# Performance work log

Measured on AMD Instinct MI355X. Metric: run time of the kernel, lower is better.

The kernel has to match this reference:

```python
import jax, jax.numpy as jnp
import numpy as np

NUM_HEADS = 16
NUM_KV_HEADS = 4
ROPE_BASE = 10000.0
TRAIN_SEQ_LEN = 2048


def _rms_norm(x):
    eps = jnp.asarray(jnp.finfo(x.dtype).eps, x.dtype)
    return x * jax.lax.rsqrt(jnp.mean(x * x, axis=-1, keepdims=True) + eps)


def _rope_cos_sin(seq_len, head_dim, dtype):
    # seq_len <= TRAIN_SEQ_LEN -> no NTK rescaling, matches Rotary buffer path
    half = head_dim // 2
    inv_freq = 1.0 / (ROPE_BASE ** (jnp.arange(0, head_dim, 2, dtype=jnp.float32) / head_dim))
    t = jnp.arange(seq_len, dtype=jnp.float32)
    freqs = jnp.outer(t, inv_freq)  # [S, half]
    cos = jnp.cos(freqs)[None, :, None, :].astype(dtype)
    sin = jnp.sin(freqs)[None, :, None, :].astype(dtype)
    return cos, sin


def _apply_rotary(x, cos, sin):
    half = x.shape[-1] // 2
    x1, x2 = x[..., :half], x[..., half:]
    return jnp.concatenate([x1 * cos + x2 * sin, -x1 * sin + x2 * cos], axis=-1)


def setup_inputs() -> dict:
    key = jax.random.key(0)
    ks = jax.random.split(key, 5)
    B, S, D = 2, 2048, 2048
    kv_dim = NUM_KV_HEADS * (D // NUM_HEADS)
    sw = 0.02
    return {
        "x": jax.random.normal(ks[0], (B, S, D), jnp.float32),
        "Wq": jax.random.normal(ks[1], (D, D), jnp.float32) * sw,
        "Wk": jax.random.normal(ks[2], (kv_dim, D), jnp.float32) * sw,
        "Wv": jax.random.normal(ks[3], (kv_dim, D), jnp.float32) * sw,
        "Wproj": jax.random.normal(ks[4], (D, D), jnp.float32) * sw,
        "q_gain": jnp.ones((NUM_HEADS,), jnp.float32),
    }


def reference(x, Wq, Wk, Wv, Wproj, q_gain):
    B, S, D = x.shape
    H, Hkv = NUM_HEADS, NUM_KV_HEADS
    hd = D // H
    r = H // Hkv

    q = (x @ Wq.T).reshape(B, S, H, hd)
    k = (x @ Wk.T).reshape(B, S, Hkv, hd)
    v = (x @ Wv.T).reshape(B, S, Hkv, hd)

    q = _rms_norm(q)
    k = _rms_norm(k)

    cos, sin = _rope_cos_sin(S, hd, q.dtype)
    q = _apply_rotary(q, cos, sin)
    k = _apply_rotary(k, cos, sin)
    q = q * q_gain.astype(q.dtype)[None, None, :, None]

    # GQA: repeat kv heads (repeat_interleave along head dim)
    k = jnp.repeat(k, r, axis=2)  # [B,S,H,hd]
    v = jnp.repeat(v, r, axis=2)

    scale = 1.0 / jnp.sqrt(jnp.asarray(hd, q.dtype))
    scores = jnp.einsum("bqhd,bkhd->bhqk", q, k) * scale
    causal = jnp.tril(jnp.ones((S, S), dtype=bool))
    scores = jnp.where(causal[None, None], scores, jnp.asarray(-jnp.inf, scores.dtype))
    attn = jax.nn.softmax(scores, axis=-1)
    y = jnp.einsum("bhqk,bkhd->bqhd", attn, v)

    return y.reshape(B, S, D) @ Wproj.T
```

## Files before the change

kernel.cpp:

```cpp
#include <hip/hip_runtime.h>

#define D_MODEL 2048
#define SEQ 2048
#define BATCH 2
#define NH 16
#define NKV 4
#define HD 128
#define KVD (NKV * HD)
#define QKVN (D_MODEL + 2 * KVD)
#define MROWS (BATCH * SEQ)

typedef __attribute__((ext_vector_type(8))) short short8;
typedef __attribute__((ext_vector_type(4))) float f32x4;

__device__ __forceinline__ unsigned short f2bf(float f) {
    union { float f; unsigned int u; } v; v.f = f;
    unsigned int r = (v.u + 0x7FFFu + ((v.u >> 16) & 1u)) >> 16;
    return (unsigned short)r;
}

__device__ __forceinline__ unsigned short f2bf_pos(float f) {
    union { float f; unsigned int u; } v; v.f = f;
    return (unsigned short)((v.u + 0x8000u) >> 16);
}

__device__ __forceinline__ float bf2f(unsigned short u) {
    union { float f; unsigned int i; } v; v.i = ((unsigned int)u) << 16;
    return v.f;
}

__device__ __forceinline__ void async16(const void* g, void* l) {
    __builtin_amdgcn_global_load_lds((const __attribute__((address_space(1))) void*)g,
                                     (__attribute__((address_space(3))) void*)l, 16, 0, 0);
}

__global__ __launch_bounds__(256) void cast_all(const float* __restrict__ x,
                                                const float* __restrict__ wq,
                                                const float* __restrict__ wk,
                                                const float* __restrict__ wv,
                                                const float* __restrict__ wp,
                                                unsigned short* __restrict__ xb,
                                                unsigned short* __restrict__ wqkv,
                                                unsigned short* __restrict__ wpb) {
    int i = blockIdx.x * 256 + threadIdx.x;
    const float4* s; ushort4* d; int j;
    if (i < 2097152)      { s = (const float4*)x;  d = (ushort4*)xb;             j = i; }
    else if (i < 3145728) { s = (const float4*)wq; d = (ushort4*)wqkv;           j = i - 2097152; }
    else if (i < 3407872) { s = (const float4*)wk; d = (ushort4*)wqkv + 1048576; j = i - 3145728; }
    else if (i < 3670016) { s = (const float4*)wv; d = (ushort4*)wqkv + 1310720; j = i - 3407872; }
    else                  { s = (const float4*)wp; d = (ushort4*)wpb;            j = i - 3670016; }
    float4 v = s[j];
    ushort4 o;
    o.x = f2bf(v.x); o.y = f2bf(v.y); o.z = f2bf(v.z); o.w = f2bf(v.w);
    d[j] = o;
}

__global__ __launch_bounds__(512) void gemm_qkv(const unsigned short* __restrict__ A,
                                                const unsigned short* __restrict__ W,
                                                const float* __restrict__ gain,
                                                unsigned short* __restrict__ qbuf,
                                                unsigned short* __restrict__ kbuf,
                                                unsigned short* __restrict__ vtb) {
    __shared__ unsigned short smem[65536];
    unsigned short* tile = smem;
    const int K = D_MODEL;
    const int tid  = threadIdx.x;
    const int lane = tid & 63;
    const int wave = tid >> 6;
    const int qm   = lane & 15;
    const int quad = lane >> 4;
    const int wr   = wave >> 2;
    const int wc   = wave & 3;
    const int lin = blockIdx.x + 12 * blockIdx.y;
    const int l2  = (lin & 7) * 24 + (lin >> 3);
    const int bx  = l2 % 12;
    const int m0  = (l2 / 12) * 256;
    const int n0 = bx * 256;

    f32x4 acc[2][2][4][2];
#pragma unroll
    for (int a = 0; a < 2; a++)
#pragma unroll
        for (int b = 0; b < 2; b++)
#pragma unroll
            for (int c = 0; c < 4; c++)
#pragma unroll
                for (int d = 0; d < 2; d++) acc[a][b][c][d] = (f32x4){0.f, 0.f, 0.f, 0.f};

    const unsigned short* Asrc = A + (size_t)(m0 + (tid >> 3)) * K + (((tid & 7) ^ ((tid >> 3) & 7)) * 8);
    const unsigned short* Bsrc = W + (size_t)(n0 + (tid >> 3)) * K + (((tid & 7) ^ ((tid >> 3) & 7)) * 8);
    const int dstg = tid * 8;
    const int ck0 = ((quad ^ (qm & 7)) * 8);
    const int ck1 = (((4 + quad) ^ (qm & 7)) * 8);
    const int arow = wr * 64 + qm;
    const int brow = wc * 32 + qm;

    short8 af[4][2], bf0[2][2], bf1[2][2];

#define STG_A(mh, bufv, kt1) \
    async16(Asrc + (size_t)((mh) * 128) * K + (kt1),      &smem[(bufv) * 16384 + (mh) * 8192 + dstg]); \
    async16(Asrc + (size_t)((mh) * 128 + 64) * K + (kt1), &smem[(bufv) * 16384 + (mh) * 8192 + 4096 + dstg]);
#define STG_B(nh, bufv, kt1) \
    async16(Bsrc + (size_t)((nh) * 128) * K + (kt1),      &smem[32768 + (bufv) * 16384 + (nh) * 8192 + dstg]); \
    async16(Bsrc + (size_t)((nh) * 128 + 64) * K + (kt1), &smem[32768 + (bufv) * 16384 + (nh) * 8192 + 4096 + dstg]);

#define RD_A(ab, mh) { \
    _Pragma("unroll") \
    for (int m = 0; m < 4; m++) { \
        af[m][0] = *(const short8*)&smem[(ab) + ((mh) * 128 + arow + m * 16) * 64 + ck0]; \
        af[m][1] = *(const short8*)&smem[(ab) + ((mh) * 128 + arow + m * 16) * 64 + ck1]; \
    } }
#define RD_B(bb, nh, dstf) { \
    _Pragma("unroll") \
    for (int n = 0; n < 2; n++) { \
        dstf[n][0] = *(const short8*)&smem[(bb) + ((nh) * 128 + brow + n * 16) * 64 + ck0]; \
        dstf[n][1] = *(const short8*)&smem[(bb) + ((nh) * 128 + brow + n * 16) * 64 + ck1]; \
    } }
#define MFMA16(mh, nh, bfr) { \
    __builtin_amdgcn_s_setprio(1); \
    _Pragma("unroll") \
    for (int m = 0; m < 4; m++) \
        _Pragma("unroll") \
        for (int n = 0; n < 2; n++) { \
            acc[mh][nh][m][n] = __builtin_amdgcn_mfma_f32_16x16x32_bf16(af[m][0], bfr[n][0], acc[mh][nh][m][n], 0, 0, 0); \
            acc[mh][nh][m][n] = __builtin_amdgcn_mfma_f32_16x16x32_bf16(af[m][1], bfr[n][1], acc[mh][nh][m][n], 0, 0, 0); \
        } \
    __builtin_amdgcn_s_setprio(0); }

#define BARv asm volatile("s_barrier" ::: "memory")
#define WV4  asm volatile("s_waitcnt vmcnt(4)" ::: "memory")
#define WV2  asm volatile("s_waitcnt vmcnt(2)" ::: "memory")
#define WV0  asm volatile("s_waitcnt vmcnt(0)" ::: "memory")

#define STEP(p, kt1) { \
     RD_A((p)*16384, 0) RD_B(32768 + (p)*16384, 0, bf0) STG_A(0, (p)^1, kt1) \
    BARv; MFMA16(0, 0, bf0) WV4; BARv; \
     RD_B(32768 + (p)*16384, 1, bf1) STG_B(0, (p)^1, kt1) \
    BARv; MFMA16(0, 1, bf1) WV4; BARv; \
     RD_A((p)*16384, 1) STG_B(1, (p)^1, kt1) \
    BARv; MFMA16(1, 0, bf0) BARv; \
     STG_A(1, (p)^1, kt1) \
    BARv; MFMA16(1, 1, bf1) WV4; BARv; \
}
#define STEPE(p) { \
    RD_A((p)*16384, 0) RD_B(32768 + (p)*16384, 0, bf0) BARv; MFMA16(0, 0, bf0) WV2; BARv; \
    RD_B(32768 + (p)*16384, 1, bf1)                    BARv; MFMA16(0, 1, bf1) WV0; BARv; \
    RD_A((p)*16384, 1)                                 BARv; MFMA16(1, 0, bf0) BARv; \
    MFMA16(1, 1, bf1) \
}

    STG_A(0, 0, 0) STG_B(0, 0, 0) STG_B(1, 0, 0) STG_A(1, 0, 0)
    WV4; BARv;

#pragma unroll 1
    for (int t2 = 0; t2 < 15; ++t2) {
        STEP(0, t2 * 128 + 64)
        STEP(1, t2 * 128 + 128)
    }
    STEP(0, 1984)
    STEPE(1)
#undef STG_A
#undef STG_B
#undef RD_A
#undef RD_B
#undef MFMA16
#undef STEP
#undef STEPE

    const int s_base = m0 & 2047;
    const int bb = m0 >> 11;
    const float invf = __builtin_amdgcn_exp2f(-(float)lane * 0.20761871f - 2.6514961f);

#pragma unroll
    for (int half = 0; half < 2; ++half) {
        __syncthreads();
#pragma unroll
        for (int nh = 0; nh < 2; nh++)
#pragma unroll
            for (int m = 0; m < 4; m++)
#pragma unroll
                for (int n = 0; n < 2; n++)
#pragma unroll
                    for (int r = 0; r < 4; r++) {
                        int row = wr * 64 + m * 16 + quad * 4 + r;
                        int col = nh * 128 + wc * 32 + n * 16 + qm;
                        tile[row * 264 + col] = f2bf(acc[half][nh][m][n][r]);
                    }
        __syncthreads();

        if (bx < 10) {
            const bool isq = bx < 8;
#pragma unroll
            for (int hh = 0; hh < 2; hh++) {
                const int h = (isq ? 2 * bx : (bx - 8) * 2) + hh;
                const float g = isq ? gain[h] * 0.12751744f : 1.0f;
                unsigned short* dst = isq
                    ? qbuf + ((size_t)(bb * NH + h) * SEQ + s_base + half * 128) * HD
                    : kbuf + ((size_t)(bb * NKV + h) * SEQ + s_base + half * 128) * HD;
                for (int rr = 0; rr < 16; rr++) {
                    int row = wave * 16 + rr;
                    float x1 = bf2f(tile[row * 264 + hh * 128 + lane]);
                    float x2 = bf2f(tile[row * 264 + hh * 128 + 64 + lane]);
                    float ss = x1 * x1 + x2 * x2;
                    ss += __shfl_xor(ss, 1);  ss += __shfl_xor(ss, 2);  ss += __shfl_xor(ss, 4);
                    ss += __shfl_xor(ss, 8);  ss += __shfl_xor(ss, 16); ss += __shfl_xor(ss, 32);
                    float rs = rsqrtf(ss * (1.0f / 128.0f) + 1.1920929e-07f);
                    float rev = (float)(s_base + half * 128 + row) * invf;
                    rev -= truncf(rev);
                    float sn = __builtin_amdgcn_sinf(rev);
                    float cs = __builtin_amdgcn_cosf(rev);
                    float a1 = x1 * rs, a2 = x2 * rs;
                    float o1 = (a1 * cs + a2 * sn) * g;
                    float o2 = (a2 * cs - a1 * sn) * g;
                    dst[(size_t)row * HD + lane]      = f2bf(o1);
                    dst[(size_t)row * HD + 64 + lane] = f2bf(o2);
                }
            }
        } else {
            const int sc = (tid & 31) * 4;
            const int d0 = tid >> 5;
#pragma unroll
            for (int hh = 0; hh < 2; hh++) {
                const int hk = (bx - 10) * 2 + hh;
                unsigned short* dstv = vtb + ((size_t)(bb * NKV + hk) * HD) * SEQ + s_base + half * 128;
#pragma unroll
                for (int i = 0; i < 8; i++) {
                    int d = d0 + 16 * i;
                    ushort4 ov;
                    ov.x = tile[(sc + 0) * 264 + hh * 128 + d];
                    ov.y = tile[(sc + 1) * 264 + hh * 128 + d];
                    ov.z = tile[(sc + 2) * 264 + hh * 128 + d];
                    ov.w = tile[(sc + 3) * 264 + hh * 128 + d];
                    *(ushort4*)(dstv + (size_t)d * SEQ + sc) = ov;
                }
            }
        }
    }
}

__global__ __launch_bounds__(256) void gemm_bt(const unsigned short* __restrict__ A,
                                               const unsigned short* __restrict__ W,
                                               float* __restrict__ C, int M, int N, int K) {
    __shared__ unsigned short smem[32768];
    unsigned short* Al = smem;
    unsigned short* Bl = smem + 16384;
    const int tid  = threadIdx.x;
    const int lane = tid & 63;
    const int wave = tid >> 6;
    const int qm   = lane & 15;
    const int quad = lane >> 4;
    const int m0 = blockIdx.y * 128;
    const int n0 = blockIdx.x * 128;
    const int wm = (wave >> 1) * 64;
    const int wn = (wave & 1) * 64;

    f32x4 acc[4][4];
#pragma unroll
    for (int i = 0; i < 4; i++)
#pragma unroll
        for (int j = 0; j < 4; j++) acc[i][j] = (f32x4){0.f, 0.f, 0.f, 0.f};

    const int r1 = tid >> 2;
    const int c1 = (((tid & 3) ^ ((tid >> 3) & 3)) * 8);
    const unsigned short* Ag = A + (size_t)(m0 + r1) * K + c1;
    const unsigned short* Wg = W + (size_t)(n0 + r1) * K + c1;
    const int stg = wave * 512;
    const int swq = ((qm >> 1) & 3) * 8;

#define STG_B2(khv, bufv) \
    async16(Ag + (khv) * 32,                  &Al[(bufv) * 8192 + (khv) * 4096 + stg]); \
    async16(Ag + (khv) * 32 + (size_t)64 * K, &Al[(bufv) * 8192 + (khv) * 4096 + 2048 + stg]); \
    async16(Wg + (khv) * 32,                  &Bl[(bufv) * 8192 + (khv) * 4096 + stg]); \
    async16(Wg + (khv) * 32 + (size_t)64 * K, &Bl[(bufv) * 8192 + (khv) * 4096 + 2048 + stg]);

#define CMP_B2(bufv, khv) { \
    short8 af[4], bfr[4]; \
    _Pragma("unroll") \
    for (int i = 0; i < 4; i++) { \
        af[i]  = *(const short8*)&Al[(bufv) * 8192 + (khv) * 4096 + (wm + i * 16 + qm) * 32 + (quad * 8 ^ swq)]; \
        bfr[i] = *(const short8*)&Bl[(bufv) * 8192 + (khv) * 4096 + (wn + i * 16 + qm) * 32 + (quad * 8 ^ swq)]; \
    } \
    __builtin_amdgcn_s_setprio(1); \
    _Pragma("unroll") \
    for (int mi = 0; mi < 4; mi++) \
        _Pragma("unroll") \
        for (int ni = 0; ni < 4; ni++) \
            acc[mi][ni] = __builtin_amdgcn_mfma_f32_16x16x32_bf16(af[mi], bfr[ni], acc[mi][ni], 0, 0, 0); \
    __builtin_amdgcn_s_setprio(0); \
}

    STG_B2(0, 0)
    STG_B2(1, 0)
    Ag += 64; Wg += 64;
    asm volatile("s_waitcnt vmcnt(4)\n\ts_barrier" ::: "memory");

    int buf = 0;
    for (int t = 0; t < K / 64 - 1; ++t) {
        STG_B2(0, buf ^ 1)
        CMP_B2(buf, 0)
        asm volatile("s_waitcnt vmcnt(4)\n\ts_barrier" ::: "memory");
        STG_B2(1, buf ^ 1)
        CMP_B2(buf, 1)
        asm volatile("s_waitcnt vmcnt(4)\n\ts_barrier" ::: "memory");
        Ag += 64; Wg += 64;
        buf ^= 1;
    }
    CMP_B2(buf, 0)
    asm volatile("s_waitcnt vmcnt(0)\n\ts_barrier" ::: "memory");
    CMP_B2(buf, 1)
#undef STG_B2
#undef CMP_B2

#pragma unroll
    for (int mi = 0; mi < 4; mi++) {
#pragma unroll
        for (int r = 0; r < 4; r++) {
            int row = m0 + wm + mi * 16 + quad * 4 + r;
            float* Crow = C + (size_t)row * N + n0 + wn + qm;
#pragma unroll
            for (int ni = 0; ni < 4; ni++) Crow[ni * 16] = acc[mi][ni][r];
        }
    }
}

__global__ __launch_bounds__(256, 4) void attn(const unsigned short* __restrict__ qb,
                                               const unsigned short* __restrict__ kb,
                                               const unsigned short* __restrict__ vt,
                                               const float* __restrict__ gain,
                                               unsigned short* __restrict__ y) {
    __shared__ unsigned short Ks[8192];
    __shared__ unsigned short Vs[8192];
    __shared__ unsigned short plds[4][1024];
    const int tid  = threadIdx.x;
    const int lane = tid & 63;
    const int wave = tid >> 6;
    const int bh   = blockIdx.x & 31;
    const int g4   = blockIdx.x >> 5;
    const int gg = g4 & 7;
    const int gs = g4 >> 3;
    const int qt64 = (gs == 0) ? gg : (gs == 1) ? (31 - gg) : (gs == 2) ? (8 + gg) : (23 - gg);
    const int h = bh & 15;
    const int b = bh >> 4;
    const int qm   = lane & 15;
    const int quad = lane >> 4;
    const int q0    = qt64 * 64;
    const int qrow0 = q0 + wave * 16;
    const float M = 17.0f * fabsf(gain[h]);

    const unsigned short* Qp = qb + (((size_t)(b * NH + h)) * SEQ + qrow0) * HD;
    const unsigned short* Kp = kb + ((size_t)(b * NKV + (h >> 2))) * SEQ * HD;
    const unsigned short* Vp = vt + ((size_t)(b * NKV + (h >> 2))) * HD * SEQ;

    short8 qf[4];
#pragma unroll
    for (int c = 0; c < 4; c++)
        qf[c] = *(const short8*)(Qp + qm * HD + c * 32 + quad * 8);

    f32x4 o[8];
#pragma unroll
    for (int t = 0; t < 8; t++) o[t] = (f32x4){0.f, 0.f, 0.f, 0.f};
    float lr[4] = {0.f, 0.f, 0.f, 0.f};

    const unsigned short* KsA = Kp + (size_t)(tid >> 4) * HD + (((tid & 15) ^ (tid >> 4)) & 15) * 8;
    const unsigned short* VsA = Vp + (size_t)(tid >> 3) * SEQ + (((tid & 7) ^ ((tid >> 3) & 7)) * 8);
    char* KsB = (char*)Ks + wave * 1024;
    char* VsB = (char*)Vs + wave * 1024;
    unsigned short* P = &plds[wave][0];

    const int kvend = q0 + 64;
    for (int kv0 = 0; kv0 < kvend; kv0 += 64) {
#pragma unroll
        for (int i = 0; i < 4; i++) {
            async16(KsA + (size_t)(16 * i) * HD,  KsB + i * 4096);
            async16(VsA + (size_t)(32 * i) * SEQ, VsB + i * 4096);
        }
        KsA += (size_t)64 * HD;
        VsA += 64;
        __syncthreads();

        f32x4 s[4];
#pragma unroll
        for (int g = 0; g < 4; g++) s[g] = (f32x4){0.f, 0.f, 0.f, 0.f};
        __builtin_amdgcn_s_setprio(1);
#pragma unroll
        for (int c = 0; c < 4; c++) {
#pragma unroll
            for (int g = 0; g < 4; g++) {
                short8 kf = *(const short8*)&Ks[(g * 16 + qm) * 128 + (((c * 4 + quad) ^ qm) * 8)];
                s[g] = __builtin_amdgcn_mfma_f32_16x16x32_bf16(qf[c], kf, s[g], 0, 0, 0);
            }
        }
        __builtin_amdgcn_s_setprio(0);
        if (kv0 + 63 > qrow0) {
#pragma unroll
            for (int g = 0; g < 4; g++)
#pragma unroll
                for (int r = 0; r < 4; r++) {
                    int qg = qrow0 + quad * 4 + r;
                    if (kv0 + g * 16 + qm > qg) s[g][r] = -3.0e38f;
                }
        }
        float p[4][4];
#pragma unroll
        for (int g = 0; g < 4; g++)
#pragma unroll
            for (int r = 0; r < 4; r++) {
                p[g][r] = __builtin_amdgcn_exp2f(s[g][r] - M);
                lr[r] += p[g][r];
            }
#pragma unroll
        for (int g = 0; g < 4; g++)
#pragma unroll
            for (int r = 0; r < 4; r++) {
                int rowp = quad * 4 + r;
                P[rowp * 64 + (((g * 2 + (qm >> 3)) ^ (rowp & 7)) * 8) + (qm & 7)] = f2bf_pos(p[g][r]);
            }
        short8 pa[2];
#pragma unroll
        for (int ka = 0; ka < 2; ka++)
            pa[ka] = *(const short8*)&P[qm * 64 + (((ka * 4 + quad) ^ (qm & 7)) * 8)];
        __builtin_amdgcn_s_setprio(1);
#pragma unroll
        for (int t = 0; t < 8; t++) {
#pragma unroll
            for (int ka = 0; ka < 2; ka++) {
                short8 vf = *(const short8*)&Vs[(t * 16 + qm) * 64 + (((ka * 4 + quad) ^ (qm & 7)) * 8)];
                o[t] = __builtin_amdgcn_mfma_f32_16x16x32_bf16(pa[ka], vf, o[t], 0, 0, 0);
            }
        }
        __builtin_amdgcn_s_setprio(0);
        __syncthreads();
    }
    float rl[4];
#pragma unroll
    for (int r = 0; r < 4; r++) {
        float l = lr[r];
        l += __shfl_xor(l, 1);
        l += __shfl_xor(l, 2);
        l += __shfl_xor(l, 4);
        l += __shfl_xor(l, 8);
        rl[r] = 1.0f / l;
    }
#pragma unroll
    for (int t = 0; t < 8; t++) {
#pragma unroll
        for (int r = 0; r < 4; r++) {
            size_t row = (size_t)(b * SEQ + qrow0 + quad * 4 + r);
            y[row * D_MODEL + h * HD + t * 16 + qm] = f2bf(o[t][r] * rl[r]);
        }
    }
}

extern "C" void kernel_launch(void* const* d_in, const int* in_sizes, int n_in,
                              void* d_out, int out_size, void* d_ws, size_t ws_size,
                              hipStream_t stream) {
    const float* x  = (const float*)d_in[0];
    const float* Wq = (const float*)d_in[1];
    const float* Wk = (const float*)d_in[2];
    const float* Wv = (const float*)d_in[3];
    const float* Wp = (const float*)d_in[4];
    const float* qg = (const float*)d_in[5];

    char* ws = (char*)d_ws;
    unsigned short* xb   = (unsigned short*)(ws + 0);
    unsigned short* wqkv = (unsigned short*)(ws + 16777216);
    unsigned short* wp   = (unsigned short*)(ws + 29360128);
    unsigned short* qbuf = (unsigned short*)(ws + 37748736);
    unsigned short* kbuf = (unsigned short*)(ws + 54525952);
    unsigned short* vtb  = (unsigned short*)(ws + 58720256);
    unsigned short* y    = xb;

    cast_all<<<18432, 256, 0, stream>>>(x, Wq, Wk, Wv, Wp, xb, wqkv, wp);
    gemm_qkv<<<dim3(12, 16), 512, 0, stream>>>(xb, wqkv, qg, qbuf, kbuf, vtb);
    attn<<<1024, 256, 0, stream>>>(qbuf, kbuf, vtb, qg, y);
    gemm_bt<<<dim3(16, 32), 256, 0, stream>>>(y, wp, (float*)d_out, MROWS, D_MODEL, D_MODEL);
}
```

Before: 280.3 us.

## Restructure output projection GEMM to 256x128 tiles with 512 threads

Rewrites the output-projection GEMM to use 256x128 block tiles with 8 waves, a K-step of 64 with XOR-swizzled LDS layout, a finer-grained interleaved async load/MFMA schedule, and a block-index remap for L2 locality. Grid shrinks from 512 to 256 blocks. The goal is more reuse of loaded operands per block and better overlap of global loads with MFMA work. In exchange it uses more LDS (96KB) and fewer blocks, which may reduce occupancy or leave CUs idle.

```diff
diff --git a/kernel.cpp b/kernel.cpp
--- a/kernel.cpp
+++ b/kernel.cpp
@@ -238,89 +238,117 @@
     }
 }
 
-__global__ __launch_bounds__(256) void gemm_bt(const unsigned short* __restrict__ A,
+__global__ __launch_bounds__(512) void gemm_bt(const unsigned short* __restrict__ A,
                                                const unsigned short* __restrict__ W,
                                                float* __restrict__ C, int M, int N, int K) {
-    __shared__ unsigned short smem[32768];
-    unsigned short* Al = smem;
-    unsigned short* Bl = smem + 16384;
+    __shared__ unsigned short smem[49152];
     const int tid  = threadIdx.x;
     const int lane = tid & 63;
     const int wave = tid >> 6;
     const int qm   = lane & 15;
     const int quad = lane >> 4;
-    const int m0 = blockIdx.y * 128;
-    const int n0 = blockIdx.x * 128;
-    const int wm = (wave >> 1) * 64;
-    const int wn = (wave & 1) * 64;
-
-    f32x4 acc[4][4];
-#pragma unroll
-    for (int i = 0; i < 4; i++)
-#pragma unroll
-        for (int j = 0; j < 4; j++) acc[i][j] = (f32x4){0.f, 0.f, 0.f, 0.f};
-
-    const int r1 = tid >> 2;
-    const int c1 = (((tid & 3) ^ ((tid >> 3) & 3)) * 8);
-    const unsigned short* Ag = A + (size_t)(m0 + r1) * K + c1;
-    const unsigned short* Wg = W + (size_t)(n0 + r1) * K + c1;
-    const int stg = wave * 512;
-    const int swq = ((qm >> 1) & 3) * 8;
-
-#define STG_B2(khv, bufv) \
-    async16(Ag + (khv) * 32,                  &Al[(bufv) * 8192 + (khv) * 4096 + stg]); \
-    async16(Ag + (khv) * 32 + (size_t)64 * K, &Al[(bufv) * 8192 + (khv) * 4096 + 2048 + stg]); \
-    async16(Wg + (khv) * 32,                  &Bl[(bufv) * 8192 + (khv) * 4096 + stg]); \
-    async16(Wg + (khv) * 32 + (size_t)64 * K, &Bl[(bufv) * 8192 + (khv) * 4096 + 2048 + stg]);
-
-#define CMP_B2(bufv, khv) { \
-    short8 af[4], bfr[4]; \
+    const int wr   = wave >> 2;
+    const int wc   = wave & 3;
+    const int lin = blockIdx.x + 16 * blockIdx.y;
+    const int l2  = (lin & 7) * 32 + (lin >> 3);
+    const int m0  = (l2 >> 4) * 256;
+    const int n0  = (l2 & 15) * 128;
+
+    f32x4 acc[2][4][2];
+#pragma unroll
+    for (int a = 0; a < 2; a++)
+#pragma unroll
+        for (int b = 0; b < 4; b++)
+#pragma unroll
+            for (int c = 0; c < 2; c++) acc[a][b][c] = (f32x4){0.f, 0.f, 0.f, 0.f};
+
+    const unsigned short* Asrc = A + (size_t)(m0 + (tid >> 3)) * K + (((tid & 7) ^ ((tid >> 3) & 7)) * 8);
+    const unsigned short* Bsrc = W + (size_t)(n0 + (tid >> 3)) * K + (((tid & 7) ^ ((tid >> 3) & 7)) * 8);
+    const int dstg = tid * 8;
+    const int ck0 = ((quad ^ (qm & 7)) * 8);
+    const int ck1 = (((4 + quad) ^ (qm & 7)) * 8);
+    const int arow = wr * 64 + qm;
+    const int brow = wc * 32 + qm;
+
+    short8 af[4][2], bfr[2][2];
+
+#define STG_A2(mh, bufv, kt1) \
+    async16(Asrc + (size_t)((mh) * 128) * K + (kt1),      &smem[(bufv) * 16384 + (mh) * 8192 + dstg]); \
+    async16(Asrc + (size_t)((mh) * 128 + 64) * K + (kt1), &smem[(bufv) * 16384 + (mh) * 8192 + 4096 + dstg]);
+#define STG_Bp(bufv, kt1) \
+    async16(Bsrc + (kt1),                  &smem[32768 + (bufv) * 8192 + dstg]); \
+    async16(Bsrc + (size_t)64 * K + (kt1), &smem[32768 + (bufv) * 8192 + 4096 + dstg]);
+
+#define RD_A2(p, mh) { \
     _Pragma("unroll") \
-    for (int i = 0; i < 4; i++) { \
-        af[i]  = *(const short8*)&Al[(bufv) * 8192 + (khv) * 4096 + (wm + i * 16 + qm) * 32 + (quad * 8 ^ swq)]; \
-        bfr[i] = *(const short8*)&Bl[(bufv) * 8192 + (khv) * 4096 + (wn + i * 16 + qm) * 32 + (quad * 8 ^ swq)]; \
-    } \
+    for (int m = 0; m < 4; m++) { \
+        af[m][0] = *(const short8*)&smem[(p) * 16384 + ((mh) * 128 + arow + m * 16) * 64 + ck0]; \
+        af[m][1] = *(const short8*)&smem[(p) * 16384 + ((mh) * 128 + arow + m * 16) * 64 + ck1]; \
+    } }
+#define RD_Bp(p) { \
+    _Pragma("unroll") \
+    for (int n = 0; n < 2; n++) { \
+        bfr[n][0] = *(const short8*)&smem[32768 + (p) * 8192 + (brow + n * 16) * 64 + ck0]; \
+        bfr[n][1] = *(const short8*)&smem[32768 + (p) * 8192 + (brow + n * 16) * 64 + ck1]; \
+    } }
+#define MFMA8(mh, kk) { \
     __builtin_amdgcn_s_setprio(1); \
     _Pragma("unroll") \
-    for (int mi = 0; mi < 4; mi++) \
+    for (int m = 0; m < 4; m++) \
         _Pragma("unroll") \
-        for (int ni = 0; ni < 4; ni++) \
-            acc[mi][ni] = __builtin_amdgcn_mfma_f32_16x16x32_bf16(af[mi], bfr[ni], acc[mi][ni], 0, 0, 0); \
-    __builtin_amdgcn_s_setprio(0); \
-}
-
-    STG_B2(0, 0)
-    STG_B2(1, 0)
-    Ag += 64; Wg += 64;
-    asm volatile("s_waitcnt vmcnt(4)\n\ts_barrier" ::: "memory");
-
-    int buf = 0;
-    for (int t = 0; t < K / 64 - 1; ++t) {
-        STG_B2(0, buf ^ 1)
-        CMP_B2(buf, 0)
-        asm volatile("s_waitcnt vmcnt(4)\n\ts_barrier" ::: "memory");
-        STG_B2(1, buf ^ 1)
-        CMP_B2(buf, 1)
-        asm volatile("s_waitcnt vmcnt(4)\n\ts_barrier" ::: "memory");
-        Ag += 64; Wg += 64;
-        buf ^= 1;
+        for (int n = 0; n < 2; n++) \
+            acc[mh][m][n] = __builtin_amdgcn_mfma_f32_16x16x32_bf16(af[m][kk], bfr[n][kk], acc[mh][m][n], 0, 0, 0); \
+    __builtin_amdgcn_s_setprio(0); }
+
+#define BARb asm volatile("s_barrier" ::: "memory")
+#define WB4  asm volatile("s_waitcnt vmcnt(4)" ::: "memory")
+#define WB2  asm volatile("s_waitcnt vmcnt(2)" ::: "memory")
+#define WB0  asm volatile("s_waitcnt vmcnt(0)" ::: "memory")
+
+#define STEPB(p, kt1) { \
+     RD_A2(p, 0) RD_Bp(p) STG_A2(0, (p)^1, kt1) \
+    BARb; MFMA8(0, 0) BARb; \
+     STG_Bp((p)^1, kt1) \
+    BARb; MFMA8(0, 1) WB4; BARb; \
+     RD_A2(p, 1) STG_A2(1, (p)^1, kt1) \
+    BARb; MFMA8(1, 0) BARb; \
+     MFMA8(1, 1) WB2; BARb; \
+}
+#define STEPBE(p) { \
+    RD_A2(p, 0) RD_Bp(p) MFMA8(0, 0) MFMA8(0, 1) \
+    WB0; BARb; \
+    RD_A2(p, 1) MFMA8(1, 0) MFMA8(1, 1) \
+}
+
+    STG_A2(0, 0, 0) STG_Bp(0, 0) STG_A2(1, 0, 0)
+    WB2; BARb;
+
+#pragma unroll 1
+    for (int t2 = 0; t2 < 15; ++t2) {
+        STEPB(0, t2 * 128 + 64)
+        STEPB(1, t2 * 128 + 128)
     }
-    CMP_B2(buf, 0)
-    asm volatile("s_waitcnt vmcnt(0)\n\ts_barrier" ::: "memory");
-    CMP_B2(buf, 1)
-#undef STG_B2
-#undef CMP_B2
-
-#pragma unroll
-    for (int mi = 0; mi < 4; mi++) {
-#pragma unroll
-        for (int r = 0; r < 4; r++) {
-            int row = m0 + wm + mi * 16 + quad * 4 + r;
-            float* Crow = C + (size_t)row * N + n0 + wn + qm;
-#pragma unroll
-            for (int ni = 0; ni < 4; ni++) Crow[ni * 16] = acc[mi][ni][r];
-        }
-    }
+    STEPB(0, 1984)
+    STEPBE(1)
+#undef STG_A2
+#undef STG_Bp
+#undef RD_A2
+#undef RD_Bp
+#undef MFMA8
+#undef STEPB
+#undef STEPBE
+
+#pragma unroll
+    for (int mh = 0; mh < 2; mh++)
+#pragma unroll
+        for (int m = 0; m < 4; m++)
+#pragma unroll
+            for (int r = 0; r < 4; r++) {
+                int row = m0 + mh * 128 + wr * 64 + m * 16 + quad * 4 + r;
+                float* Crow = C + (size_t)row * N + n0 + wc * 32 + qm;
+#pragma unroll
+                for (int n = 0; n < 2; n++) Crow[n * 16] = acc[mh][m][n][r];
+            }
 }
 
 __global__ __launch_bounds__(256, 4) void attn(const unsigned short* __restrict__ qb,
@@ -473,5 +501,5 @@
     cast_all<<<18432, 256, 0, stream>>>(x, Wq, Wk, Wv, Wp, xb, wqkv, wp);
     gemm_qkv<<<dim3(12, 16), 512, 0, stream>>>(xb, wqkv, qg, qbuf, kbuf, vtb);
     attn<<<1024, 256, 0, stream>>>(qbuf, kbuf, vtb, qg, y);
-    gemm_bt<<<dim3(16, 32), 256, 0, stream>>>(y, wp, (float*)d_out, MROWS, D_MODEL, D_MODEL);
-}
+    gemm_bt<<<dim3(16, 16), 512, 0, stream>>>(y, wp, (float*)d_out, MROWS, D_MODEL, D_MODEL);
+}
```

Measured after the change: 275.1 us. Within noise of the previous version (-1.9%).
